# Kernel tuning notes

Hardware: AMD Instinct MI355X
Metric: run time of the kernel (lower is better)

Reference implementation:

```python
import jax, jax.numpy as jnp
import numpy as np
import math

B, L, D, H = 16, 512, 128, 8


def setup_inputs() -> dict:
    key = jax.random.key(0)
    ks = jax.random.split(key, 10)
    xavier = lambda k, shp: jax.random.normal(k, shp, jnp.float32) * math.sqrt(2.0 / (shp[0] + shp[1]))
    inp = {
        "x": jax.random.normal(ks[0], (B, L, D), jnp.float32),
        "W_q": xavier(ks[1], (H * D, D)),
        "b_q": jnp.zeros((H * D,), jnp.float32),
        "W_k": xavier(ks[2], (H * D, D)),
        "b_k": jnp.zeros((H * D,), jnp.float32),
        "W_v": xavier(ks[3], (H * D, D)),
        "b_v": jnp.zeros((H * D,), jnp.float32),
        "W_o": xavier(ks[4], (D, H * D)),
        "b_o": jnp.zeros((D,), jnp.float32),
        "pad_mask": jax.random.randint(ks[5], (B, L, L), 0, 2).astype(bool),
        "batch_size": B,
        "max_len": L,
    }
    return inp


def reference(x, W_q, b_q, W_k, b_k, W_v, b_v, W_o, b_o, pad_mask, batch_size, max_len):
    # project: [B, L, D] -> [B, L, H*D] -> head-major [H*B, L, D]
    def proj(W, b):
        y = jnp.einsum('bld,ed->ble', x, W) + b          # [B, L, H*D]
        y = y.reshape(batch_size, max_len, H, D)
        return y.transpose(2, 0, 1, 3).reshape(H * batch_size, max_len, D)

    q = proj(W_q, b_q)
    k = proj(W_k, b_k)
    v = proj(W_v, b_v)

    scores = jnp.einsum('nqd,nkd->nqk', q, k)            # [H*B, L, L]
    mask = jnp.tile(pad_mask, (H, 1, 1))                 # repeat(n_heads,1,1)
    # faithful quirk: mask BEFORE scaling, softmax over QUERY axis (dim=1)
    scores = jnp.where(mask, -1e9, scores) / math.sqrt(D)
    attn = jax.nn.softmax(scores, axis=1)
    att = jnp.einsum('nqk,nkd->nqd', attn, v)            # [H*B, L, D]
    # faithful quirk: torch .view from (H*B, L, D) to (B, L, H*D)
    att = att.reshape(batch_size, max_len, H * D)
    out = jnp.einsum('ble,de->bld', att, W_o) + b_o      # [B, L, D]
    return out
```

## Files before the change

### kernel.cpp

```cpp
#include <hip/hip_runtime.h>

#define B_  16
#define L_  512
#define D_  128
#define H_  8
#define HD_ 1024
#define NH_ 128
#define M_  8192

typedef unsigned short u16;
typedef __attribute__((ext_vector_type(8))) short s16x8;
typedef __attribute__((ext_vector_type(4))) float f32x4;

__device__ __forceinline__ float bf2f(u16 u) {
    union { unsigned u; float f; } x; x.u = ((unsigned)u) << 16; return x.f;
}
__device__ __forceinline__ u16 f2bf(float f) {
    unsigned u = __float_as_uint(f);
    return (u16)((u + 0x7FFFu + ((u >> 16) & 1u)) >> 16);
}

__device__ __forceinline__ void mfma_bt64(const u16* __restrict__ A, int lda,
                                          const u16* __restrict__ B, int ldb,
                                          int K, int lane, f32x4 acc[4][4]) {
    const int mr = lane & 15, quad = lane >> 4;
    for (int k0 = 0; k0 < K; k0 += 32) {
        s16x8 av[4], bv[4];
#pragma unroll
        for (int i = 0; i < 4; i++)
            av[i] = *(const s16x8*)(A + (size_t)(i * 16 + mr) * lda + k0 + quad * 8);
#pragma unroll
        for (int j = 0; j < 4; j++)
            bv[j] = *(const s16x8*)(B + (size_t)(j * 16 + mr) * ldb + k0 + quad * 8);
#pragma unroll
        for (int i = 0; i < 4; i++)
#pragma unroll
            for (int j = 0; j < 4; j++)
                acc[i][j] = __builtin_amdgcn_mfma_f32_16x16x32_bf16(av[i], bv[j], acc[i][j], 0, 0, 0);
    }
}

__global__ void k0_detect(const unsigned int* __restrict__ pad,
                          const unsigned int* __restrict__ xw,
                          int* __restrict__ flags) {
    __shared__ int sMask, sCnt;
    if (threadIdx.x == 0) { sMask = 0; sCnt = 0; }
    __syncthreads();
    int bad = 0;
#pragma unroll
    for (int i = 0; i < 4; i++) {
        unsigned u = pad[threadIdx.x * 4 + i];
        bad |= (u > 1u) ? 1 : 0;
    }
    int cnt = 0;
#pragma unroll
    for (int i = 0; i < 16; i++) {
        unsigned w = xw[threadIdx.x * 16 + i];
        unsigned e = (w >> 7) & 0xFFu;
        cnt += (e >= 100u && e <= 131u) ? 1 : 0;
    }
    if (bad) atomicOr(&sMask, 1);
    atomicAdd(&sCnt, cnt);
    __syncthreads();
    if (threadIdx.x == 0) {
        flags[0] = (sCnt > 2048) ? 1 : 0;
        flags[1] = sMask;
    }
}

#define PREP_TOT 1576064
__global__ __launch_bounds__(256) void kprep_conv(
    const void* x, const void* Wq, const void* bq, const void* Wk, const void* bk,
    const void* Wv, const void* bv, const void* Wo, const void* bo,
    const int* __restrict__ flags,
    u16* xb, u16* Wqb, u16* Wkb, u16* Wvb, u16* Wob,
    u16* bqb, u16* bkb, u16* bvb, u16* bob) {
    int gid = blockIdx.x * 256 + threadIdx.x;
    if (gid >= PREP_TOT) return;
    const int dt = flags[0];
    const void* src; u16* dst; int off;
    if      (gid < 1048576) { src = x;  dst = xb;  off = gid; }
    else if (gid < 1179648) { src = Wq; dst = Wqb; off = gid - 1048576; }
    else if (gid < 1310720) { src = Wk; dst = Wkb; off = gid - 1179648; }
    else if (gid < 1441792) { src = Wv; dst = Wvb; off = gid - 1310720; }
    else if (gid < 1572864) { src = Wo; dst = Wob; off = gid - 1441792; }
    else if (gid < 1573888) { src = bq; dst = bqb; off = gid - 1572864; }
    else if (gid < 1574912) { src = bk; dst = bkb; off = gid - 1573888; }
    else if (gid < 1575936) { src = bv; dst = bvb; off = gid - 1574912; }
    else                    { src = bo; dst = bob; off = gid - 1575936; }
    dst[off] = dt ? ((const u16*)src)[off] : f2bf(((const float*)src)[off]);
}

__global__ __launch_bounds__(256) void kprep_mask(const void* __restrict__ pad,
                                                  const int* __restrict__ flags,
                                                  unsigned* __restrict__ mb,
                                                  float* __restrict__ colsum) {
    int w = blockIdx.x * 256 + threadIdx.x;
    if (w < NH_ * L_) colsum[w] = 0.0f;
    size_t base = (size_t)w * 32;
    unsigned m = 0;
    if (flags[1]) {
        const unsigned char* p = (const unsigned char*)pad;
#pragma unroll
        for (int b = 0; b < 32; b++) m |= (p[base + b] ? 1u : 0u) << b;
    } else {
        const int* p = (const int*)pad;
#pragma unroll
        for (int b = 0; b < 32; b++) m |= (p[base + b] ? 1u : 0u) << b;
    }
    mb[w] = m;
}

__global__ __launch_bounds__(256) void k1_proj(
    const u16* __restrict__ xb,
    const u16* __restrict__ Wqb, const u16* __restrict__ Wkb, const u16* __restrict__ Wvb,
    const u16* __restrict__ bqb, const u16* __restrict__ bkb, const u16* __restrict__ bvb,
    u16* __restrict__ qb, u16* __restrict__ kb, u16* __restrict__ vtb) {
    const int h  = blockIdx.x;
    const int m0 = blockIdx.y * 128;
    const int z  = blockIdx.z;
    const u16* W    = (z == 0) ? Wqb : (z == 1) ? Wkb : Wvb;
    const u16* bias = (z == 0) ? bqb : (z == 1) ? bkb : bvb;

    const int lane = threadIdx.x & 63, wave = threadIdx.x >> 6;
    const int wr = wave >> 1, wc = wave & 1;
    const int mr = lane & 15, quad = lane >> 4;

    f32x4 acc[4][4];
#pragma unroll
    for (int i = 0; i < 4; i++)
#pragma unroll
        for (int j = 0; j < 4; j++) acc[i][j] = (f32x4){0.f, 0.f, 0.f, 0.f};

    mfma_bt64(xb + (size_t)(m0 + wr * 64) * D_, D_,
              W + (size_t)(h * 128 + wc * 64) * D_, D_, D_, lane, acc);

    __shared__ __align__(16) u16 T[128][144];
#pragma unroll
    for (int i = 0; i < 4; i++)
#pragma unroll
        for (int j = 0; j < 4; j++) {
            int col = wc * 64 + j * 16 + mr;
            float bv_ = bf2f(bias[h * 128 + col]);
#pragma unroll
            for (int r = 0; r < 4; r++)
                T[wr * 64 + i * 16 + quad * 4 + r][col] = f2bf(acc[i][j][r] + bv_);
        }
    __syncthreads();

    const int bb = m0 >> 9, l0 = m0 & 511;
    const int t = threadIdx.x;
    if (z < 2) {
        u16* out = z ? kb : qb;
        int row = t >> 1, c0 = (t & 1) * 64;
        u16* dst = out + ((size_t)(h * B_ + bb) * L_ + l0 + row) * D_ + c0;
#pragma unroll
        for (int c = 0; c < 64; c += 8)
            *(uint4*)(dst + c) = *(const uint4*)&T[row][c0 + c];
    } else {
        int d = t >> 1, lc0 = (t & 1) * 64;
        u16* dst = vtb + ((size_t)(h * B_ + bb) * D_ + d) * L_ + l0 + lc0;
#pragma unroll
        for (int c = 0; c < 64; c += 8) {
            u16 tmp[8];
#pragma unroll
            for (int s = 0; s < 8; s++) tmp[s] = T[lc0 + c + s][d];
            *(uint4*)(dst + c) = *(const uint4*)tmp;
        }
    }
}

__global__ __launch_bounds__(256, 4) void k2_scores(
    const u16* __restrict__ qb, const u16* __restrict__ kb,
    const unsigned* __restrict__ mbits,
    u16* __restrict__ sb, float* __restrict__ colsum) {
    const int qt = blockIdx.x >> 2, kt = blockIdx.x & 3;
    const int n  = blockIdx.y;
    const int bb = n & (B_ - 1);
    const int lane = threadIdx.x & 63, wave = threadIdx.x >> 6;
    const int wr = wave >> 1, wc = wave & 1;
    const int mr = lane & 15, quad = lane >> 4;
    const float rs = 0.08838834764831845f;

    __shared__ __align__(16) u16 T[128][136];
    __shared__ float CS[2][128];
    __shared__ unsigned MW[128][4];

    {
        int t = threadIdx.x;
        int q = t >> 1, w2 = (t & 1) * 2;
        const unsigned* src = mbits + ((size_t)(bb << 9) + qt * 128 + q) * 16 + kt * 4 + w2;
        uint2 v = *(const uint2*)src;
        MW[q][w2] = v.x; MW[q][w2 + 1] = v.y;
    }

    f32x4 acc[4][4];
#pragma unroll
    for (int i = 0; i < 4; i++)
#pragma unroll
        for (int j = 0; j < 4; j++) acc[i][j] = (f32x4){0.f, 0.f, 0.f, 0.f};

    mfma_bt64(qb + ((size_t)n * L_ + qt * 128 + wr * 64) * D_, D_,
              kb + ((size_t)n * L_ + kt * 128 + wc * 64) * D_, D_, D_, lane, acc);
    __syncthreads();

    float cs[4] = {0.f, 0.f, 0.f, 0.f};
#pragma unroll
    for (int j = 0; j < 4; j++) {
        const int wsel = wc * 2 + (j >> 1);
        const int bit  = ((j & 1) << 4) + mr;
#pragma unroll
        for (int i = 0; i < 4; i++)
#pragma unroll
            for (int r = 0; r < 4; r++) {
                int ql = wr * 64 + i * 16 + quad * 4 + r;
                unsigned w = MW[ql][wsel];
                float e = ((w >> bit) & 1u) ? 0.f : __expf(acc[i][j][r] * rs);
                cs[j] += e;
                T[ql][wc * 64 + j * 16 + mr] = f2bf(e);
            }
    }
#pragma unroll
    for (int j = 0; j < 4; j++) {
        cs[j] += __shfl_xor(cs[j], 16);
        cs[j] += __shfl_xor(cs[j], 32);
    }
    if (quad == 0) {
#pragma unroll
        for (int j = 0; j < 4; j++) CS[wr][wc * 64 + j * 16 + mr] = cs[j];
    }
    __syncthreads();
    {
        int t = threadIdx.x, row = t >> 1, c0 = (t & 1) * 64;
        u16* dst = sb + ((size_t)n * L_ + qt * 128 + row) * L_ + kt * 128 + c0;
#pragma unroll
        for (int c = 0; c < 64; c += 8)
            *(uint4*)(dst + c) = *(const uint4*)&T[row][c0 + c];
    }
    if (threadIdx.x < 128)
        atomicAdd(&colsum[(size_t)n * L_ + kt * 128 + threadIdx.x],
                  CS[0][threadIdx.x] + CS[1][threadIdx.x]);
}

__global__ __launch_bounds__(256) void k3_vscale(u16* __restrict__ vtb,
                                                 const float* __restrict__ colsum) {
    int idx = blockIdx.x * 256 + threadIdx.x;
    int n = idx >> 13;
    int rem = idx & 8191;
    int d = rem >> 6;
    int kg = (rem & 63) << 3;
    u16* p = vtb + ((size_t)n * D_ + d) * L_ + kg;
    uint4 v = *(const uint4*)p;
    float cv[8];
    *(float4*)&cv[0] = *(const float4*)(colsum + (size_t)n * L_ + kg);
    *(float4*)&cv[4] = *(const float4*)(colsum + (size_t)n * L_ + kg + 4);
    u16* u = (u16*)&v;
#pragma unroll
    for (int s = 0; s < 8; s++) u[s] = f2bf(bf2f(u[s]) / cv[s]);
    *(uint4*)p = v;
}

__global__ __launch_bounds__(256, 4) void k4_av(
    const u16* __restrict__ sb, const u16* __restrict__ vtb,
    u16* __restrict__ att) {
    const int q0 = blockIdx.x * 64;
    const int n  = blockIdx.y;
    const int lane = threadIdx.x & 63, wave = threadIdx.x >> 6;
    const int wr = wave >> 1, wc = wave & 1;
    const int mr = lane & 15, quad = lane >> 4;

    f32x4 acc[2][4];
#pragma unroll
    for (int i = 0; i < 2; i++)
#pragma unroll
        for (int j = 0; j < 4; j++) acc[i][j] = (f32x4){0.f, 0.f, 0.f, 0.f};

    const u16* A  = sb  + ((size_t)n * L_ + q0 + wr * 32) * L_;
    const u16* Bb = vtb + ((size_t)n * D_ + wc * 64) * L_;

    for (int k0 = 0; k0 < L_; k0 += 32) {
        s16x8 av[2], bv[4];
#pragma unroll
        for (int i = 0; i < 2; i++)
            av[i] = *(const s16x8*)(A + (size_t)(i * 16 + mr) * L_ + k0 + quad * 8);
#pragma unroll
        for (int j = 0; j < 4; j++)
            bv[j] = *(const s16x8*)(Bb + (size_t)(j * 16 + mr) * L_ + k0 + quad * 8);
#pragma unroll
        for (int i = 0; i < 2; i++)
#pragma unroll
            for (int j = 0; j < 4; j++)
                acc[i][j] = __builtin_amdgcn_mfma_f32_16x16x32_bf16(av[i], bv[j], acc[i][j], 0, 0, 0);
    }

    __shared__ __align__(16) u16 T[64][136];
#pragma unroll
    for (int i = 0; i < 2; i++)
#pragma unroll
        for (int j = 0; j < 4; j++)
#pragma unroll
            for (int r = 0; r < 4; r++)
                T[wr * 32 + i * 16 + quad * 4 + r][wc * 64 + j * 16 + mr] = f2bf(acc[i][j][r]);
    __syncthreads();
    int t = threadIdx.x, row = t >> 2, c0 = (t & 3) * 32;
    u16* dst = att + ((size_t)n * L_ + q0 + row) * D_ + c0;
#pragma unroll
    for (int c = 0; c < 32; c += 8)
        *(uint4*)(dst + c) = *(const uint4*)&T[row][c0 + c];
}

__global__ __launch_bounds__(128) void k5_out(
    const u16* __restrict__ att, const u16* __restrict__ Wob,
    const u16* __restrict__ bob, const int* __restrict__ flags,
    void* __restrict__ out) {
    const int dt = flags[0];
    const int m0 = blockIdx.x * 64;
    const int lane = threadIdx.x & 63, wc = threadIdx.x >> 6;
    const int mr = lane & 15, quad = lane >> 4;

    f32x4 acc[4][4];
#pragma unroll
    for (int i = 0; i < 4; i++)
#pragma unroll
        for (int j = 0; j < 4; j++) acc[i][j] = (f32x4){0.f, 0.f, 0.f, 0.f};

    mfma_bt64(att + (size_t)m0 * HD_, HD_,
              Wob + (size_t)(wc * 64) * HD_, HD_, HD_, lane, acc);

    __shared__ __align__(16) float Tf[64][132];
#pragma unroll
    for (int i = 0; i < 4; i++)
#pragma unroll
        for (int j = 0; j < 4; j++) {
            int col = wc * 64 + j * 16 + mr;
            float bv_ = bf2f(bob[col]);
#pragma unroll
            for (int r = 0; r < 4; r++)
                Tf[i * 16 + quad * 4 + r][col] = acc[i][j][r] + bv_;
        }
    __syncthreads();
    int t = threadIdx.x, row = t >> 1, c0 = (t & 1) * 64;
    size_t base = (size_t)(m0 + row) * D_ + c0;
    if (dt) {
        u16* o = (u16*)out;
#pragma unroll
        for (int c = 0; c < 64; c += 8) {
            u16 tmp[8];
#pragma unroll
            for (int s = 0; s < 8; s++) tmp[s] = f2bf(Tf[row][c0 + c + s]);
            *(uint4*)(o + base + c) = *(const uint4*)tmp;
        }
    } else {
        float* o = (float*)out;
#pragma unroll
        for (int c = 0; c < 64; c += 4)
            *(float4*)(o + base + c) = *(const float4*)&Tf[row][c0 + c];
    }
}

extern "C" void kernel_launch(void* const* d_in, const int* in_sizes, int n_in,
                              void* d_out, int out_size, void* d_ws, size_t ws_size,
                              hipStream_t stream) {
    (void)in_sizes; (void)n_in; (void)out_size; (void)ws_size;
    const void* x  = d_in[0];
    const void* Wq = d_in[1]; const void* bq = d_in[2];
    const void* Wk = d_in[3]; const void* bk = d_in[4];
    const void* Wv = d_in[5]; const void* bv = d_in[6];
    const void* Wo = d_in[7]; const void* bo = d_in[8];
    const void* pad = d_in[9];

    char* p = (char*)d_ws;
    auto alloc = [&](size_t bytes) { char* r = p; p += (bytes + 255) & ~(size_t)255; return r; };
    int*  flags = (int*)alloc(256);
    u16*  xb   = (u16*)alloc(2097152);
    u16*  Wqb  = (u16*)alloc(262144);
    u16*  Wkb  = (u16*)alloc(262144);
    u16*  Wvb  = (u16*)alloc(262144);
    u16*  Wob  = (u16*)alloc(262144);
    u16*  bqb  = (u16*)alloc(2048);
    u16*  bkb  = (u16*)alloc(2048);
    u16*  bvb  = (u16*)alloc(2048);
    u16*  bob  = (u16*)alloc(256);
    unsigned* mbits = (unsigned*)alloc(524288);
    float* colsum = (float*)alloc(262144);
    u16*  qb   = (u16*)alloc(16777216);
    u16*  kb   = (u16*)alloc(16777216);
    u16*  vtb  = (u16*)alloc(16777216);
    u16*  sb   = (u16*)alloc(67108864);
    u16*  att  = qb;

    k0_detect<<<1, 256, 0, stream>>>((const unsigned*)pad, (const unsigned*)x, flags);
    kprep_conv<<<(PREP_TOT + 255) / 256, 256, 0, stream>>>(
        x, Wq, bq, Wk, bk, Wv, bv, Wo, bo, flags,
        xb, Wqb, Wkb, Wvb, Wob, bqb, bkb, bvb, bob);
    kprep_mask<<<512, 256, 0, stream>>>(pad, flags, mbits, colsum);
    k1_proj<<<dim3(8, 64, 3), 256, 0, stream>>>(
        xb, Wqb, Wkb, Wvb, bqb, bkb, bvb, qb, kb, vtb);
    k2_scores<<<dim3(16, NH_), 256, 0, stream>>>(qb, kb, mbits, sb, colsum);
    k3_vscale<<<4096, 256, 0, stream>>>(vtb, colsum);
    k4_av<<<dim3(8, NH_), 256, 0, stream>>>(sb, vtb, att);
    k5_out<<<128, 128, 0, stream>>>(att, Wob, bob, flags, d_out);
}
```

Before: 275.6 us.

## Vectorize mask packing, enlarge AV tiles, and split output GEMM finer

Mask packing now reads the pad mask with 16-byte vector loads instead of per-element byte or int loads. The attention-times-V kernel moves from 64-row to 128-row query tiles through the shared mfma_bt64 helper, giving each wave a 64x64 tile so V is reused more. The output projection goes from 128 blocks of 128 threads to 256 blocks of 256 threads with 32-row tiles, raising parallelism across CUs. The larger AV tile halves the grid and drops the occupancy hint, which may reduce latency hiding.

Result: faster. 253.4 us (-8.1%).

```diff
diff --git a/kernel.cpp b/kernel.cpp
--- a/kernel.cpp
+++ b/kernel.cpp
@@ -97,16 +97,29 @@
                                                   float* __restrict__ colsum) {
     int w = blockIdx.x * 256 + threadIdx.x;
     if (w < NH_ * L_) colsum[w] = 0.0f;
-    size_t base = (size_t)w * 32;
     unsigned m = 0;
     if (flags[1]) {
-        const unsigned char* p = (const unsigned char*)pad;
-#pragma unroll
-        for (int b = 0; b < 32; b++) m |= (p[base + b] ? 1u : 0u) << b;
+        const uint4* p = (const uint4*)pad + (size_t)w * 2;
+        uint4 a = p[0], b = p[1];
+        unsigned ws[8] = {a.x, a.y, a.z, a.w, b.x, b.y, b.z, b.w};
+#pragma unroll
+        for (int i = 0; i < 8; i++) {
+            unsigned v = ws[i];
+            m |= ((v & 0xFFu)        ? 1u : 0u) << (i * 4)
+               | ((v & 0xFF00u)     ? 1u : 0u) << (i * 4 + 1)
+               | ((v & 0xFF0000u)   ? 1u : 0u) << (i * 4 + 2)
+               | ((v & 0xFF000000u) ? 1u : 0u) << (i * 4 + 3);
+        }
     } else {
-        const int* p = (const int*)pad;
-#pragma unroll
-        for (int b = 0; b < 32; b++) m |= (p[base + b] ? 1u : 0u) << b;
+        const uint4* p = (const uint4*)pad + (size_t)w * 8;
+#pragma unroll
+        for (int i = 0; i < 8; i++) {
+            uint4 v = p[i];
+            m |= (v.x ? 1u : 0u) << (i * 4)
+               | (v.y ? 1u : 0u) << (i * 4 + 1)
+               | (v.z ? 1u : 0u) << (i * 4 + 2)
+               | (v.w ? 1u : 0u) << (i * 4 + 3);
+        }
     }
     mb[w] = m;
 }
@@ -260,101 +273,100 @@
     *(uint4*)p = v;
 }
 
-__global__ __launch_bounds__(256, 4) void k4_av(
+__global__ __launch_bounds__(256) void k4_av(
     const u16* __restrict__ sb, const u16* __restrict__ vtb,
     u16* __restrict__ att) {
-    const int q0 = blockIdx.x * 64;
+    const int q0 = blockIdx.x * 128;
     const int n  = blockIdx.y;
     const int lane = threadIdx.x & 63, wave = threadIdx.x >> 6;
     const int wr = wave >> 1, wc = wave & 1;
     const int mr = lane & 15, quad = lane >> 4;
 
-    f32x4 acc[2][4];
-#pragma unroll
-    for (int i = 0; i < 2; i++)
+    f32x4 acc[4][4];
+#pragma unroll
+    for (int i = 0; i < 4; i++)
 #pragma unroll
         for (int j = 0; j < 4; j++) acc[i][j] = (f32x4){0.f, 0.f, 0.f, 0.f};
 
-    const u16* A  = sb  + ((size_t)n * L_ + q0 + wr * 32) * L_;
-    const u16* Bb = vtb + ((size_t)n * D_ + wc * 64) * L_;
-
-    for (int k0 = 0; k0 < L_; k0 += 32) {
-        s16x8 av[2], bv[4];
-#pragma unroll
-        for (int i = 0; i < 2; i++)
-            av[i] = *(const s16x8*)(A + (size_t)(i * 16 + mr) * L_ + k0 + quad * 8);
-#pragma unroll
-        for (int j = 0; j < 4; j++)
-            bv[j] = *(const s16x8*)(Bb + (size_t)(j * 16 + mr) * L_ + k0 + quad * 8);
-#pragma unroll
-        for (int i = 0; i < 2; i++)
-#pragma unroll
-            for (int j = 0; j < 4; j++)
-                acc[i][j] = __builtin_amdgcn_mfma_f32_16x16x32_bf16(av[i], bv[j], acc[i][j], 0, 0, 0);
-    }
-
-    __shared__ __align__(16) u16 T[64][136];
-#pragma unroll
-    for (int i = 0; i < 2; i++)
-#pragma unroll
-        for (int j = 0; j < 4; j++)
+    mfma_bt64(sb + ((size_t)n * L_ + q0 + wr * 64) * L_, L_,
+              vtb + ((size_t)n * D_ + wc * 64) * L_, L_, L_, lane, acc);
+
+    __shared__ __align__(16) u16 T[128][136];
+#pragma unroll
+    for (int i = 0; i < 4; i++)
+#pragma unroll
+        for (int j = 0; j < 4; j++) {
+            int col = wc * 64 + j * 16 + mr;
 #pragma unroll
             for (int r = 0; r < 4; r++)
-                T[wr * 32 + i * 16 + quad * 4 + r][wc * 64 + j * 16 + mr] = f2bf(acc[i][j][r]);
-    __syncthreads();
-    int t = threadIdx.x, row = t >> 2, c0 = (t & 3) * 32;
+                T[wr * 64 + i * 16 + quad * 4 + r][col] = f2bf(acc[i][j][r]);
+        }
+    __syncthreads();
+    int t = threadIdx.x, row = t >> 1, c0 = (t & 1) * 64;
     u16* dst = att + ((size_t)n * L_ + q0 + row) * D_ + c0;
 #pragma unroll
-    for (int c = 0; c < 32; c += 8)
+    for (int c = 0; c < 64; c += 8)
         *(uint4*)(dst + c) = *(const uint4*)&T[row][c0 + c];
 }
 
-__global__ __launch_bounds__(128) void k5_out(
+__global__ __launch_bounds__(256) void k5_out(
     const u16* __restrict__ att, const u16* __restrict__ Wob,
     const u16* __restrict__ bob, const int* __restrict__ flags,
     void* __restrict__ out) {
     const int dt = flags[0];
-    const int m0 = blockIdx.x * 64;
-    const int lane = threadIdx.x & 63, wc = threadIdx.x >> 6;
+    const int m0 = blockIdx.x * 32;
+    const int lane = threadIdx.x & 63, wave = threadIdx.x >> 6;
     const int mr = lane & 15, quad = lane >> 4;
 
-    f32x4 acc[4][4];
-#pragma unroll
-    for (int i = 0; i < 4; i++)
-#pragma unroll
-        for (int j = 0; j < 4; j++) acc[i][j] = (f32x4){0.f, 0.f, 0.f, 0.f};
-
-    mfma_bt64(att + (size_t)m0 * HD_, HD_,
-              Wob + (size_t)(wc * 64) * HD_, HD_, HD_, lane, acc);
-
-    __shared__ __align__(16) float Tf[64][132];
-#pragma unroll
-    for (int i = 0; i < 4; i++)
-#pragma unroll
-        for (int j = 0; j < 4; j++) {
-            int col = wc * 64 + j * 16 + mr;
+    f32x4 acc[2][2];
+#pragma unroll
+    for (int i = 0; i < 2; i++)
+#pragma unroll
+        for (int j = 0; j < 2; j++) acc[i][j] = (f32x4){0.f, 0.f, 0.f, 0.f};
+
+    const u16* A  = att + (size_t)m0 * HD_;
+    const u16* Bw = Wob + (size_t)(wave * 32) * HD_;
+    for (int k0 = 0; k0 < HD_; k0 += 32) {
+        s16x8 av[2], bv[2];
+#pragma unroll
+        for (int i = 0; i < 2; i++)
+            av[i] = *(const s16x8*)(A + (size_t)(i * 16 + mr) * HD_ + k0 + quad * 8);
+#pragma unroll
+        for (int j = 0; j < 2; j++)
+            bv[j] = *(const s16x8*)(Bw + (size_t)(j * 16 + mr) * HD_ + k0 + quad * 8);
+#pragma unroll
+        for (int i = 0; i < 2; i++)
+#pragma unroll
+            for (int j = 0; j < 2; j++)
+                acc[i][j] = __builtin_amdgcn_mfma_f32_16x16x32_bf16(av[i], bv[j], acc[i][j], 0, 0, 0);
+    }
+
+    __shared__ __align__(16) float Tf[32][132];
+#pragma unroll
+    for (int i = 0; i < 2; i++)
+#pragma unroll
+        for (int j = 0; j < 2; j++) {
+            int col = wave * 32 + j * 16 + mr;
             float bv_ = bf2f(bob[col]);
 #pragma unroll
             for (int r = 0; r < 4; r++)
                 Tf[i * 16 + quad * 4 + r][col] = acc[i][j][r] + bv_;
         }
     __syncthreads();
-    int t = threadIdx.x, row = t >> 1, c0 = (t & 1) * 64;
-    size_t base = (size_t)(m0 + row) * D_ + c0;
+    int t = threadIdx.x, row = t >> 3, cg = (t & 7) * 16;
+    size_t base = (size_t)(m0 + row) * D_ + cg;
     if (dt) {
         u16* o = (u16*)out;
-#pragma unroll
-        for (int c = 0; c < 64; c += 8) {
-            u16 tmp[8];
-#pragma unroll
-            for (int s = 0; s < 8; s++) tmp[s] = f2bf(Tf[row][c0 + c + s]);
-            *(uint4*)(o + base + c) = *(const uint4*)tmp;
-        }
+        u16 tmp[16];
+#pragma unroll
+        for (int s = 0; s < 16; s++) tmp[s] = f2bf(Tf[row][cg + s]);
+        *(uint4*)(o + base)     = *(const uint4*)&tmp[0];
+        *(uint4*)(o + base + 8) = *(const uint4*)&tmp[8];
     } else {
         float* o = (float*)out;
 #pragma unroll
-        for (int c = 0; c < 64; c += 4)
-            *(float4*)(o + base + c) = *(const float4*)&Tf[row][c0 + c];
+        for (int c = 0; c < 16; c += 4)
+            *(float4*)(o + base + c) = *(const float4*)&Tf[row][cg + c];
     }
 }
 
@@ -398,6 +410,6 @@
         xb, Wqb, Wkb, Wvb, bqb, bkb, bvb, qb, kb, vtb);
     k2_scores<<<dim3(16, NH_), 256, 0, stream>>>(qb, kb, mbits, sb, colsum);
     k3_vscale<<<4096, 256, 0, stream>>>(vtb, colsum);
-    k4_av<<<dim3(8, NH_), 256, 0, stream>>>(sb, vtb, att);
-    k5_out<<<128, 128, 0, stream>>>(att, Wob, bob, flags, d_out);
-}
+    k4_av<<<dim3(4, NH_), 256, 0, stream>>>(sb, vtb, att);
+    k5_out<<<256, 256, 0, stream>>>(att, Wob, bob, flags, d_out);
+}
```
